# Kernel optimization log

Measured on AMD Instinct MI355X. Metric: run time of the kernel, lower is better.

The kernel has to match this reference:

```python
import jax, jax.numpy as jnp
import numpy as np

B, T, D = 2, 1024, 2048
N, K, H = 16, 4, 128          # num_heads, num_kv_heads, head_dim
TC = 1024                     # cached tokens
S = TC + T
MAX_WAVELENGTH = 10000.0
BIG_NEG = -2.3819763e38


def _apply_rope(x, positions):
    """RoPE: positions [B,L] applied to x [B,L,heads,H]."""
    half = x.shape[-1] // 2
    freq_exponents = (2.0 / x.shape[-1]) * jnp.arange(half, dtype=jnp.float32)
    timescale = MAX_WAVELENGTH ** freq_exponents                      # [H/2]
    radians = (positions.astype(jnp.float32)[..., None] / timescale)[..., None, :]  # [B,L,1,H/2]
    sin, cos = jnp.sin(radians), jnp.cos(radians)
    x1, x2 = jnp.split(x, 2, axis=-1)
    res = jnp.concatenate([x1 * cos - x2 * sin, x2 * cos + x1 * sin], axis=-1)
    return res.astype(x.dtype)


def setup_inputs() -> dict:
    key = jax.random.key(0)
    ks = jax.random.split(key, 8)
    x = jax.random.normal(ks[0], (B, T, D), dtype=jnp.float32)
    # new tokens sit right after the cache
    positions = jnp.broadcast_to(TC + jnp.arange(T, dtype=jnp.int32), (B, T))
    # causal mask over [cache + new]: query t may attend to keys s <= TC + t
    s_idx = jnp.arange(S)[None, :]
    t_idx = jnp.arange(T)[:, None]
    attn_mask = jnp.broadcast_to((s_idx <= TC + t_idx)[None, None, :, :], (B, 1, T, S))
    cache_k = jax.random.normal(ks[1], (B, TC, K, H), dtype=jnp.float32)
    cache_v = jax.random.normal(ks[2], (B, TC, K, H), dtype=jnp.float32)
    # lecun-normal-ish fan-in scaling (fan_in = D for projections, N*H for output)
    w_q = jax.random.normal(ks[3], (N, D, H), dtype=jnp.float32) * (D ** -0.5)
    w_kv = jax.random.normal(ks[4], (2, K, D, H), dtype=jnp.float32) * (D ** -0.5)
    w_out = jax.random.normal(ks[5], (N, H, D), dtype=jnp.float32) * ((N * H) ** -0.5)
    return {"x": x, "positions": positions, "attn_mask": attn_mask,
            "cache_k": cache_k, "cache_v": cache_v,
            "w_q": w_q, "w_kv": w_kv, "w_out": w_out}


def reference(x, positions, attn_mask, cache_k, cache_v, w_q, w_kv, w_out):
    dtype = x.dtype
    # projections (GQA path: num_kv_heads != num_heads)
    q = jnp.einsum('BTD,NDH->BTNH', x, w_q.astype(dtype))
    kv = jnp.einsum('BSD,CKDH->CBSKH', x, w_kv.astype(dtype))
    k_new, v_new = kv[0], kv[1]
    # inline RoPE + query scaling
    q = _apply_rope(q, positions) * (H ** -0.5)
    k_new = _apply_rope(k_new, positions)
    # KV-cache concat
    k = jnp.concatenate([cache_k, k_new], axis=1)   # [B,S,K,H]
    v = jnp.concatenate([cache_v, v_new], axis=1)
    # group heads: B T (K G) H -> B T K G H
    G = N // K
    qg = q.reshape(q.shape[0], q.shape[1], K, G, H)
    logits = jnp.einsum('BTKGH,BSKH->BKGTS', qg, k,
                        preferred_element_type=jnp.float32)
    masked = jnp.where(attn_mask[:, :, None, :, :], logits, BIG_NEG)
    probs = jax.nn.softmax(masked, axis=-1).astype(dtype)
    enc = jnp.einsum('BKGTS,BSKH->BTKGH', probs, v)
    enc = enc.reshape(enc.shape[0], enc.shape[1], N, H)  # B T (K G) H
    out = jnp.einsum('BTNH,NHD->BTD', enc, w_out.astype(dtype))
    return out, k, v
```

## Files before the change

### kernel.cpp

```cpp
#include <hip/hip_runtime.h>

#define B_  2
#define T_  1024
#define D_  2048
#define NH  16
#define KH  4
#define HD  128
#define TC_ 1024
#define S_  2048

typedef __bf16 bf16x4v __attribute__((ext_vector_type(4)));
typedef __bf16 bf16x8v __attribute__((ext_vector_type(8)));
typedef float  f32x4v  __attribute__((ext_vector_type(4)));

__device__ __forceinline__ void async_copy16(void* lds, const void* g) {
    __builtin_amdgcn_global_load_lds(
        (__attribute__((address_space(1))) void*)g,
        (__attribute__((address_space(3))) void*)lds, 16, 0, 0);
}

__global__ void prep(const float* __restrict__ x, __bf16* __restrict__ xb,
                     const float4* __restrict__ ck, const float4* __restrict__ cv,
                     float* __restrict__ kout, float* __restrict__ vout,
                     __bf16* __restrict__ kb) {
    int bid = blockIdx.x;
    if (bid < 4096) {
        int i = (bid * 256 + threadIdx.x) * 4;
        float4 v = *(const float4*)(x + i);
        bf16x4v o; o[0]=(__bf16)v.x; o[1]=(__bf16)v.y; o[2]=(__bf16)v.z; o[3]=(__bf16)v.w;
        *(bf16x4v*)(xb + i) = o;
    } else {
        int i = (bid - 4096) * 256 + threadIdx.x;
        int b = i >> 17;
        int r = i & 131071;
        float4 kv = ck[i];
        ((float4*)(kout + (size_t)b * S_ * KH * HD))[r] = kv;
        ((float4*)(vout + (size_t)b * S_ * KH * HD))[r] = cv[i];
        int h4 = r & 31;
        int kh = (r >> 5) & 3;
        int s  = r >> 7;
        bf16x4v o; o[0]=(__bf16)kv.x; o[1]=(__bf16)kv.y; o[2]=(__bf16)kv.z; o[3]=(__bf16)kv.w;
        *(bf16x4v*)(kb + (((size_t)(b * KH + kh) * S_ + s) * HD) + h4 * 4) = o;
    }
}

__global__ void tp_all(const float* __restrict__ wq, const float* __restrict__ wkv,
                       const float* __restrict__ wo, __bf16* __restrict__ wt,
                       __bf16* __restrict__ wot) {
    __shared__ float tile[32][33];
    int bid = blockIdx.x;
    int tx = threadIdx.x, ty = threadIdx.y;
    if (bid < 6144) {
        int zz  = bid >> 8;
        int rem = bid & 255;
        int h0 = (rem & 3) * 32;
        int d0 = (rem >> 2) * 32;
        const float* ip = (zz < 16) ? (wq + (size_t)zz * D_ * HD)
                                    : (wkv + (size_t)(zz - 16) * D_ * HD);
        __bf16* op = wt + (size_t)zz * D_ * HD;
        for (int i = 0; i < 32; i += 8)
            tile[ty + i][tx] = ip[(size_t)(d0 + ty + i) * HD + h0 + tx];
        __syncthreads();
        for (int i = 0; i < 32; i += 8)
            op[(size_t)(h0 + ty + i) * D_ + d0 + tx] = (__bf16)tile[tx][ty + i];
    } else {
        int r2  = bid - 6144;
        int n   = r2 >> 8;
        int rem = r2 & 255;
        int d0 = (rem & 63) * 32;
        int h0 = (rem >> 6) * 32;
        const float* ip = wo + (size_t)n * (HD * D_);
        for (int i = 0; i < 32; i += 8)
            tile[ty + i][tx] = ip[(size_t)(h0 + ty + i) * D_ + d0 + tx];
        __syncthreads();
        for (int i = 0; i < 32; i += 8)
            wot[(size_t)(d0 + ty + i) * (NH * HD) + n * HD + h0 + tx] = (__bf16)tile[tx][ty + i];
    }
}

__global__ void tp_v(const float* __restrict__ vout, __bf16* __restrict__ vtb) {
    __shared__ float tile[32][33];
    int z = blockIdx.z; int b = z / KH, kh = z % KH;
    int h0 = blockIdx.x * 32;
    int s0 = blockIdx.y * 32;
    const float* ip = vout + ((size_t)b * S_ * KH + kh) * HD;
    int tx = threadIdx.x, ty = threadIdx.y;
    for (int i = 0; i < 32; i += 8)
        tile[ty + i][tx] = ip[(size_t)(s0 + ty + i) * (KH * HD) + h0 + tx];
    __syncthreads();
    __bf16* op = vtb + ((size_t)b * KH + kh) * (size_t)HD * S_;
    for (int i = 0; i < 32; i += 8)
        op[(size_t)(h0 + ty + i) * S_ + s0 + tx] = (__bf16)tile[tx][ty + i];
}

__global__ __launch_bounds__(256, 2)
void gemm_qkv(const __bf16* __restrict__ A, const __bf16* __restrict__ BT,
              const int* __restrict__ pos, __bf16* __restrict__ qws,
              float* __restrict__ kout, float* __restrict__ vout,
              __bf16* __restrict__ kb) {
    __shared__ __bf16 As[128 * 64];
    __shared__ __bf16 Bs[128 * 64];
    const int swz = (blockIdx.x & 7) * 48 + (blockIdx.x >> 3);
    const int m0 = (swz & 15) * 128;
    const int head = swz >> 4;
    const int n0 = head * 128;
    const int tid = threadIdx.x;
    const int wave = tid >> 6, lane = tid & 63;
    const int quad = lane >> 4, l16 = lane & 15;
    const int wm = (wave & 1) * 64;
    const int bn0 = (wave >> 1) * 32;
    const int lrow = lane >> 3;
    const int lsw  = (lane & 7) ^ (lrow & 7);

    f32x4v acc[4][4];
    for (int i = 0; i < 4; i++)
        for (int j = 0; j < 4; j++)
            acc[i][j] = (f32x4v){0.f, 0.f, 0.f, 0.f};

    const __bf16* Abase = A + (size_t)m0 * D_;
    const __bf16* Bbase = BT + (size_t)n0 * D_;

    for (int k0 = 0; k0 < D_; k0 += 64) {
        for (int j = 0; j < 4; j++) {
            int r = wave * 32 + j * 8;
            async_copy16(As + (size_t)r * 64,
                         Abase + (size_t)(r + lrow) * D_ + k0 + lsw * 8);
            async_copy16(Bs + (size_t)r * 64,
                         Bbase + (size_t)(r + lrow) * D_ + k0 + lsw * 8);
        }
        __syncthreads();
        for (int ks = 0; ks < 2; ks++) {
            const int ch = ((ks * 4 + quad) ^ (l16 & 7)) * 8;
            bf16x8v a[4], b[4];
            for (int i = 0; i < 4; i++)
                a[i] = *(const bf16x8v*)(As + (wm + i * 16 + l16) * 64 + ch);
            for (int j = 0; j < 4; j++) {
                int bn = bn0 + (j >> 1) * 16 + (j & 1) * 64;
                b[j] = *(const bf16x8v*)(Bs + (bn + l16) * 64 + ch);
            }
            for (int i = 0; i < 4; i++)
                for (int j = 0; j < 4; j++)
                    acc[i][j] = __builtin_amdgcn_mfma_f32_16x16x32_bf16(a[i], b[j], acc[i][j], 0, 0, 0);
        }
        __syncthreads();
    }

    const float RFREQ = 9.210340371976184f / 64.0f;
    const float qscale = 0.08838834764831845f;

    if (head < NH) {
        for (int i = 0; i < 4; i++)
            for (int r = 0; r < 4; r++) {
                int row = m0 + wm + i * 16 + quad * 4 + r;
                float p = (float)pos[row];
                size_t qo = ((size_t)row * NH + head) * HD;
                for (int jp = 0; jp < 2; jp++) {
                    int hh = bn0 + jp * 16 + l16;
                    float ang = p * __expf(-(float)hh * RFREQ);
                    float sn, cs; __sincosf(ang, &sn, &cs);
                    float x1 = acc[i][jp * 2][r], x2 = acc[i][jp * 2 + 1][r];
                    qws[qo + hh]      = (__bf16)((x1 * cs - x2 * sn) * qscale);
                    qws[qo + hh + 64] = (__bf16)((x2 * cs + x1 * sn) * qscale);
                }
            }
    } else if (head < NH + KH) {
        int kh = head - NH;
        for (int i = 0; i < 4; i++)
            for (int r = 0; r < 4; r++) {
                int row = m0 + wm + i * 16 + quad * 4 + r;
                int b = row >> 10, t = row & 1023;
                float p = (float)pos[row];
                size_t ko  = ((size_t)(b * S_ + TC_ + t) * KH + kh) * HD;
                size_t kbo = ((size_t)(b * KH + kh) * S_ + TC_ + t) * HD;
                for (int jp = 0; jp < 2; jp++) {
                    int hh = bn0 + jp * 16 + l16;
                    float ang = p * __expf(-(float)hh * RFREQ);
                    float sn, cs; __sincosf(ang, &sn, &cs);
                    float x1 = acc[i][jp * 2][r], x2 = acc[i][jp * 2 + 1][r];
                    float k1 = x1 * cs - x2 * sn, k2 = x2 * cs + x1 * sn;
                    kout[ko + hh]      = k1;
                    kout[ko + hh + 64] = k2;
                    kb[kbo + hh]      = (__bf16)k1;
                    kb[kbo + hh + 64] = (__bf16)k2;
                }
            }
    } else {
        int kh = head - NH - KH;
        for (int i = 0; i < 4; i++)
            for (int r = 0; r < 4; r++) {
                int row = m0 + wm + i * 16 + quad * 4 + r;
                int b = row >> 10, t = row & 1023;
                size_t vo = ((size_t)(b * S_ + TC_ + t) * KH + kh) * HD;
                for (int j = 0; j < 4; j++) {
                    int h = bn0 + (j >> 1) * 16 + (j & 1) * 64 + l16;
                    vout[vo + h] = acc[i][j][r];
                }
            }
    }
}

__global__ __launch_bounds__(256, 2)
void gemm_bt(const __bf16* __restrict__ A, const __bf16* __restrict__ BT,
             float* __restrict__ C, int ldc) {
    __shared__ __bf16 As[128 * 64];
    __shared__ __bf16 Bs[128 * 64];
    const int swz = (blockIdx.x & 7) * 32 + (blockIdx.x >> 3);
    const int m0 = (swz & 15) * 128, n0 = (swz >> 4) * 128;
    const int tid = threadIdx.x;
    const int wave = tid >> 6, lane = tid & 63;
    const int quad = lane >> 4, l16 = lane & 15;
    const int wm = (wave & 1) * 64, wn = (wave >> 1) * 64;
    const int lrow = lane >> 3;
    const int lsw  = (lane & 7) ^ (lrow & 7);

    f32x4v acc[4][4];
    for (int i = 0; i < 4; i++)
        for (int j = 0; j < 4; j++)
            acc[i][j] = (f32x4v){0.f, 0.f, 0.f, 0.f};

    const __bf16* Abase = A + (size_t)m0 * D_;
    const __bf16* Bbase = BT + (size_t)n0 * D_;

    for (int k0 = 0; k0 < D_; k0 += 64) {
        for (int j = 0; j < 4; j++) {
            int r = wave * 32 + j * 8;
            async_copy16(As + (size_t)r * 64,
                         Abase + (size_t)(r + lrow) * D_ + k0 + lsw * 8);
            async_copy16(Bs + (size_t)r * 64,
                         Bbase + (size_t)(r + lrow) * D_ + k0 + lsw * 8);
        }
        __syncthreads();
        for (int ks = 0; ks < 2; ks++) {
            const int ch = ((ks * 4 + quad) ^ (l16 & 7)) * 8;
            bf16x8v a[4], b[4];
            for (int i = 0; i < 4; i++)
                a[i] = *(const bf16x8v*)(As + (wm + i * 16 + l16) * 64 + ch);
            for (int j = 0; j < 4; j++)
                b[j] = *(const bf16x8v*)(Bs + (wn + j * 16 + l16) * 64 + ch);
            for (int i = 0; i < 4; i++)
                for (int j = 0; j < 4; j++)
                    acc[i][j] = __builtin_amdgcn_mfma_f32_16x16x32_bf16(a[i], b[j], acc[i][j], 0, 0, 0);
        }
        __syncthreads();
    }
    for (int i = 0; i < 4; i++)
        for (int j = 0; j < 4; j++)
            for (int r = 0; r < 4; r++) {
                int row = m0 + wm + i * 16 + quad * 4 + r;
                int col = n0 + wn + j * 16 + l16;
                C[(size_t)row * ldc + col] = acc[i][j][r];
            }
}

__global__ __launch_bounds__(512, 1)
void attn(const __bf16* __restrict__ qws, const __bf16* __restrict__ kb,
          const __bf16* __restrict__ vtb, __bf16* __restrict__ enc) {
    __shared__ __bf16 Qs[128 * 128];
    __shared__ __bf16 Ks[128 * 128];
    __shared__ __bf16 Vs[128 * 128];
    __shared__ __bf16 Ps[128 * 128];

    const int t0 = blockIdx.x * 128;
    const int n  = blockIdx.y;
    const int b  = blockIdx.z;
    const int kh = n / (NH / KH);
    const int tid = threadIdx.x, wave = tid >> 6, lane = tid & 63;
    const int quad = lane >> 4, l16 = lane & 15;
    const int wm = wave * 16;
    const int arow = lane >> 4;
    const int acol = lane & 15;

    {
        const __bf16* qtile = qws + ((size_t)(b * T_ + t0) * NH + n) * HD;
        for (int jj = 0; jj < 4; jj++) {
            int r0 = wm + jj * 4;
            int row = r0 + arow;
            async_copy16(Qs + (size_t)r0 * 128,
                         qtile + (size_t)row * (NH * HD) + ((acol ^ (row & 15)) * 8));
        }
    }

    float m_run[4], l_run[4];
    f32x4v o_acc[8];
    for (int r = 0; r < 4; r++) { m_run[r] = -INFINITY; l_run[r] = 0.f; }
    for (int j = 0; j < 8; j++) o_acc[j] = (f32x4v){0.f, 0.f, 0.f, 0.f};

    const int nS = (TC_ + t0 + 128) >> 7;
    const __bf16* kbase = kb  + ((size_t)(b * KH + kh)) * S_ * HD;
    const __bf16* vbase = vtb + ((size_t)(b * KH + kh)) * (size_t)HD * S_;

    for (int st = 0; st < nS; st++) {
        const int s0 = st * 128;
        {
            const __bf16* ktile = kbase + (size_t)s0 * HD;
            for (int jj = 0; jj < 4; jj++) {
                int r0 = wm + jj * 4;
                int row = r0 + arow;
                async_copy16(Ks + (size_t)r0 * 128,
                             ktile + (size_t)row * HD + ((acol ^ (row & 15)) * 8));
            }
        }
        {
            const __bf16* vtile = vbase + s0;
            for (int jj = 0; jj < 4; jj++) {
                int r0 = wm + jj * 4;
                int row = r0 + arow;
                async_copy16(Vs + (size_t)r0 * 128,
                             vtile + (size_t)row * S_ + ((acol ^ (row & 15)) * 8));
            }
        }
        __syncthreads();

        f32x4v sc[8];
        for (int j = 0; j < 8; j++) sc[j] = (f32x4v){0.f, 0.f, 0.f, 0.f};
        for (int ks = 0; ks < 4; ks++) {
            int ch = (ks * 4 + quad) ^ l16;
            bf16x8v a = *(const bf16x8v*)(Qs + (wm + l16) * 128 + ch * 8);
            bf16x8v bb[8];
            for (int j = 0; j < 8; j++)
                bb[j] = *(const bf16x8v*)(Ks + (j * 16 + l16) * 128 + ch * 8);
            for (int j = 0; j < 8; j++)
                sc[j] = __builtin_amdgcn_mfma_f32_16x16x32_bf16(a, bb[j], sc[j], 0, 0, 0);
        }

        if (st == nS - 1) {
            for (int j = 0; j < 8; j++)
                for (int r = 0; r < 4; r++) {
                    int row = wm + quad * 4 + r;
                    int col = j * 16 + l16;
                    if (col > row) sc[j][r] = -3.0e38f;
                }
        }

        for (int r = 0; r < 4; r++) {
            float mx = sc[0][r];
            for (int j = 1; j < 8; j++) mx = fmaxf(mx, sc[j][r]);
            for (int off = 8; off >= 1; off >>= 1) mx = fmaxf(mx, __shfl_xor(mx, off, 64));
            mx = fmaxf(mx, m_run[r]);
            float alpha = __expf(m_run[r] - mx);
            m_run[r] = mx;
            float s = 0.f;
            for (int j = 0; j < 8; j++) {
                float pv = __expf(sc[j][r] - mx);
                sc[j][r] = pv;
                s += pv;
            }
            for (int off = 8; off >= 1; off >>= 1) s += __shfl_xor(s, off, 64);
            l_run[r] = l_run[r] * alpha + s;
            for (int j = 0; j < 8; j++) o_acc[j][r] *= alpha;
        }

        for (int j = 0; j < 8; j++)
            for (int r = 0; r < 4; r++) {
                int row = wm + quad * 4 + r;
                int c = (j * 2 + (l16 >> 3)) ^ (row & 15);
                Ps[row * 128 + c * 8 + (l16 & 7)] = (__bf16)sc[j][r];
            }
        __syncthreads();

        for (int ks = 0; ks < 4; ks++) {
            int ch = (ks * 4 + quad) ^ l16;
            bf16x8v a = *(const bf16x8v*)(Ps + (wm + l16) * 128 + ch * 8);
            bf16x8v bb[8];
            for (int j = 0; j < 8; j++)
                bb[j] = *(const bf16x8v*)(Vs + (j * 16 + l16) * 128 + ch * 8);
            for (int j = 0; j < 8; j++)
                o_acc[j] = __builtin_amdgcn_mfma_f32_16x16x32_bf16(a, bb[j], o_acc[j], 0, 0, 0);
        }
        __syncthreads();
    }

    for (int r = 0; r < 4; r++) {
        float inv = 1.0f / l_run[r];
        int row = wm + quad * 4 + r;
        for (int j = 0; j < 8; j++) {
            int col = j * 16 + l16;
            enc[((size_t)(b * T_ + t0 + row) * NH + n) * HD + col] =
                (__bf16)(o_acc[j][r] * inv);
        }
    }
}

extern "C" void kernel_launch(void* const* d_in, const int* in_sizes, int n_in,
                              void* d_out, int out_size, void* d_ws, size_t ws_size,
                              hipStream_t stream) {
    const float* x       = (const float*)d_in[0];
    const int*   pos     = (const int*)d_in[1];
    const float* cache_k = (const float*)d_in[3];
    const float* cache_v = (const float*)d_in[4];
    const float* w_q     = (const float*)d_in[5];
    const float* w_kv    = (const float*)d_in[6];
    const float* w_out   = (const float*)d_in[7];

    float* out  = (float*)d_out;
    float* kout = out  + (size_t)B_ * T_ * D_;
    float* vout = kout + (size_t)B_ * S_ * KH * HD;

    char* ws = (char*)d_ws;
    __bf16* xb   = (__bf16*)ws;  ws += (size_t)B_ * T_ * D_ * 2;
    __bf16* wt   = (__bf16*)ws;  ws += (size_t)3072 * D_ * 2;
    __bf16* wot  = (__bf16*)ws;  ws += (size_t)D_ * NH * HD * 2;
    __bf16* qws  = (__bf16*)ws;  ws += (size_t)B_ * T_ * NH * HD * 2;
    __bf16* kbuf = (__bf16*)ws;  ws += (size_t)B_ * S_ * KH * HD * 2;
    __bf16* vtb  = (__bf16*)ws;  ws += (size_t)B_ * S_ * KH * HD * 2;
    __bf16* enc  = (__bf16*)ws;

    prep<<<5120, 256, 0, stream>>>(x, xb, (const float4*)cache_k, (const float4*)cache_v,
                                   kout, vout, kbuf);
    tp_all<<<10240, dim3(32, 8), 0, stream>>>(w_q, w_kv, w_out, wt, wot);
    gemm_qkv<<<384, 256, 0, stream>>>(xb, wt, pos, qws, kout, vout, kbuf);
    tp_v<<<dim3(4, 64, 8), dim3(32, 8), 0, stream>>>(vout, vtb);
    attn<<<dim3(8, 16, 2), 512, 0, stream>>>(qws, kbuf, vtb, enc);
    gemm_bt<<<256, 256, 0, stream>>>(enc, wot, out, 2048);
}
```

Baseline: 272.7 us.

## Merge prep, weight transposes and cached-V transpose into one kernel; emit new V^T from GEMM

Combines the input conversion, cache copy, weight transposes and the cached-V transpose into a single launch, which cuts two kernel launches and their gaps. The transposed bf16 V for new tokens is now written directly from the QKV GEMM epilogue, so the separate tp_v pass that reread the fp32 V output is gone. The cached-V transpose now reads cache_v directly instead of the freshly written output. The cost is a larger branchy prep kernel and strided 8-byte stores of V^T in the GEMM epilogue.

```diff
diff --git a/kernel.cpp b/kernel.cpp
--- a/kernel.cpp
+++ b/kernel.cpp
@@ -19,18 +19,25 @@
         (__attribute__((address_space(3))) void*)lds, 16, 0, 0);
 }
 
-__global__ void prep(const float* __restrict__ x, __bf16* __restrict__ xb,
-                     const float4* __restrict__ ck, const float4* __restrict__ cv,
-                     float* __restrict__ kout, float* __restrict__ vout,
-                     __bf16* __restrict__ kb) {
-    int bid = blockIdx.x;
+__global__ void prep_all(const float* __restrict__ x, __bf16* __restrict__ xb,
+                         const float4* __restrict__ ck, const float4* __restrict__ cv,
+                         float* __restrict__ kout, float* __restrict__ vout,
+                         __bf16* __restrict__ kb,
+                         const float* __restrict__ wq, const float* __restrict__ wkv,
+                         const float* __restrict__ wo, __bf16* __restrict__ wt,
+                         __bf16* __restrict__ wot, __bf16* __restrict__ vtb) {
+    __shared__ float tile[32][33];
+    const int bid = blockIdx.x;
+    const int tx = threadIdx.x, ty = threadIdx.y;
+    const int tid = ty * 32 + tx;
+
     if (bid < 4096) {
-        int i = (bid * 256 + threadIdx.x) * 4;
+        int i = (bid * 256 + tid) * 4;
         float4 v = *(const float4*)(x + i);
         bf16x4v o; o[0]=(__bf16)v.x; o[1]=(__bf16)v.y; o[2]=(__bf16)v.z; o[3]=(__bf16)v.w;
         *(bf16x4v*)(xb + i) = o;
-    } else {
-        int i = (bid - 4096) * 256 + threadIdx.x;
+    } else if (bid < 5120) {
+        int i = (bid - 4096) * 256 + tid;
         int b = i >> 17;
         int r = i & 131071;
         float4 kv = ck[i];
@@ -41,63 +48,56 @@
         int s  = r >> 7;
         bf16x4v o; o[0]=(__bf16)kv.x; o[1]=(__bf16)kv.y; o[2]=(__bf16)kv.z; o[3]=(__bf16)kv.w;
         *(bf16x4v*)(kb + (((size_t)(b * KH + kh) * S_ + s) * HD) + h4 * 4) = o;
-    }
-}
-
-__global__ void tp_all(const float* __restrict__ wq, const float* __restrict__ wkv,
-                       const float* __restrict__ wo, __bf16* __restrict__ wt,
-                       __bf16* __restrict__ wot) {
-    __shared__ float tile[32][33];
-    int bid = blockIdx.x;
-    int tx = threadIdx.x, ty = threadIdx.y;
-    if (bid < 6144) {
-        int zz  = bid >> 8;
-        int rem = bid & 255;
+    } else if (bid < 15360) {
+        int b2 = bid - 5120;
+        if (b2 < 6144) {
+            int zz  = b2 >> 8;
+            int rem = b2 & 255;
+            int h0 = (rem & 3) * 32;
+            int d0 = (rem >> 2) * 32;
+            const float* ip = (zz < 16) ? (wq + (size_t)zz * D_ * HD)
+                                        : (wkv + (size_t)(zz - 16) * D_ * HD);
+            __bf16* op = wt + (size_t)zz * D_ * HD;
+            for (int i = 0; i < 32; i += 8)
+                tile[ty + i][tx] = ip[(size_t)(d0 + ty + i) * HD + h0 + tx];
+            __syncthreads();
+            for (int i = 0; i < 32; i += 8)
+                op[(size_t)(h0 + ty + i) * D_ + d0 + tx] = (__bf16)tile[tx][ty + i];
+        } else {
+            int r2  = b2 - 6144;
+            int n   = r2 >> 8;
+            int rem = r2 & 255;
+            int d0 = (rem & 63) * 32;
+            int h0 = (rem >> 6) * 32;
+            const float* ip = wo + (size_t)n * (HD * D_);
+            for (int i = 0; i < 32; i += 8)
+                tile[ty + i][tx] = ip[(size_t)(h0 + ty + i) * D_ + d0 + tx];
+            __syncthreads();
+            for (int i = 0; i < 32; i += 8)
+                wot[(size_t)(d0 + ty + i) * (NH * HD) + n * HD + h0 + tx] = (__bf16)tile[tx][ty + i];
+        }
+    } else {
+        int c = bid - 15360;
+        int z = c >> 7;
+        int rem = c & 127;
         int h0 = (rem & 3) * 32;
-        int d0 = (rem >> 2) * 32;
-        const float* ip = (zz < 16) ? (wq + (size_t)zz * D_ * HD)
-                                    : (wkv + (size_t)(zz - 16) * D_ * HD);
-        __bf16* op = wt + (size_t)zz * D_ * HD;
+        int s0 = (rem >> 2) * 32;
+        int b = z >> 2, kh = z & 3;
+        const float* ip = (const float*)cv + ((size_t)b * TC_ * KH + kh) * HD;
         for (int i = 0; i < 32; i += 8)
-            tile[ty + i][tx] = ip[(size_t)(d0 + ty + i) * HD + h0 + tx];
-        __syncthreads();
+            tile[ty + i][tx] = ip[(size_t)(s0 + ty + i) * (KH * HD) + h0 + tx];
+        __syncthreads();
+        __bf16* op = vtb + ((size_t)(b * KH + kh)) * (size_t)HD * S_;
         for (int i = 0; i < 32; i += 8)
-            op[(size_t)(h0 + ty + i) * D_ + d0 + tx] = (__bf16)tile[tx][ty + i];
-    } else {
-        int r2  = bid - 6144;
-        int n   = r2 >> 8;
-        int rem = r2 & 255;
-        int d0 = (rem & 63) * 32;
-        int h0 = (rem >> 6) * 32;
-        const float* ip = wo + (size_t)n * (HD * D_);
-        for (int i = 0; i < 32; i += 8)
-            tile[ty + i][tx] = ip[(size_t)(h0 + ty + i) * D_ + d0 + tx];
-        __syncthreads();
-        for (int i = 0; i < 32; i += 8)
-            wot[(size_t)(d0 + ty + i) * (NH * HD) + n * HD + h0 + tx] = (__bf16)tile[tx][ty + i];
-    }
-}
-
-__global__ void tp_v(const float* __restrict__ vout, __bf16* __restrict__ vtb) {
-    __shared__ float tile[32][33];
-    int z = blockIdx.z; int b = z / KH, kh = z % KH;
-    int h0 = blockIdx.x * 32;
-    int s0 = blockIdx.y * 32;
-    const float* ip = vout + ((size_t)b * S_ * KH + kh) * HD;
-    int tx = threadIdx.x, ty = threadIdx.y;
-    for (int i = 0; i < 32; i += 8)
-        tile[ty + i][tx] = ip[(size_t)(s0 + ty + i) * (KH * HD) + h0 + tx];
-    __syncthreads();
-    __bf16* op = vtb + ((size_t)b * KH + kh) * (size_t)HD * S_;
-    for (int i = 0; i < 32; i += 8)
-        op[(size_t)(h0 + ty + i) * S_ + s0 + tx] = (__bf16)tile[tx][ty + i];
+            op[(size_t)(h0 + ty + i) * S_ + s0 + tx] = (__bf16)tile[tx][ty + i];
+    }
 }
 
 __global__ __launch_bounds__(256, 2)
 void gemm_qkv(const __bf16* __restrict__ A, const __bf16* __restrict__ BT,
               const int* __restrict__ pos, __bf16* __restrict__ qws,
               float* __restrict__ kout, float* __restrict__ vout,
-              __bf16* __restrict__ kb) {
+              __bf16* __restrict__ kb, __bf16* __restrict__ vtb) {
     __shared__ __bf16 As[128 * 64];
     __shared__ __bf16 Bs[128 * 64];
     const int swz = (blockIdx.x & 7) * 48 + (blockIdx.x >> 3);
@@ -186,9 +186,11 @@
             }
     } else {
         int kh = head - NH - KH;
-        for (int i = 0; i < 4; i++)
+        for (int i = 0; i < 4; i++) {
+            int row0 = m0 + wm + i * 16 + quad * 4;
+            int b0 = row0 >> 10, tb = row0 & 1023;
             for (int r = 0; r < 4; r++) {
-                int row = m0 + wm + i * 16 + quad * 4 + r;
+                int row = row0 + r;
                 int b = row >> 10, t = row & 1023;
                 size_t vo = ((size_t)(b * S_ + TC_ + t) * KH + kh) * HD;
                 for (int j = 0; j < 4; j++) {
@@ -196,6 +198,13 @@
                     vout[vo + h] = acc[i][j][r];
                 }
             }
+            for (int j = 0; j < 4; j++) {
+                int h = bn0 + (j >> 1) * 16 + (j & 1) * 64 + l16;
+                bf16x4v tv;
+                for (int r = 0; r < 4; r++) tv[r] = (__bf16)acc[i][j][r];
+                *(bf16x4v*)(vtb + ((size_t)(b0 * KH + kh) * HD + h) * S_ + TC_ + tb) = tv;
+            }
+        }
     }
 }
 
@@ -405,11 +414,10 @@
     __bf16* vtb  = (__bf16*)ws;  ws += (size_t)B_ * S_ * KH * HD * 2;
     __bf16* enc  = (__bf16*)ws;
 
-    prep<<<5120, 256, 0, stream>>>(x, xb, (const float4*)cache_k, (const float4*)cache_v,
-                                   kout, vout, kbuf);
-    tp_all<<<10240, dim3(32, 8), 0, stream>>>(w_q, w_kv, w_out, wt, wot);
-    gemm_qkv<<<384, 256, 0, stream>>>(xb, wt, pos, qws, kout, vout, kbuf);
-    tp_v<<<dim3(4, 64, 8), dim3(32, 8), 0, stream>>>(vout, vtb);
+    prep_all<<<16384, dim3(32, 8), 0, stream>>>(x, xb, (const float4*)cache_k,
+                                                (const float4*)cache_v, kout, vout, kbuf,
+                                                w_q, w_kv, w_out, wt, wot, vtb);
+    gemm_qkv<<<384, 256, 0, stream>>>(xb, wt, pos, qws, kout, vout, kbuf, vtb);
     attn<<<dim3(8, 16, 2), 512, 0, stream>>>(qws, kbuf, vtb, enc);
     gemm_bt<<<256, 256, 0, stream>>>(enc, wot, out, 2048);
 }
```

New measurement: 266.6 us. 2.2% less time.
